# Performance work log

Measured on AMD Instinct MI355X. Metric: run time of the kernel, lower is better.

Reference implementation:

```python
import jax, jax.numpy as jnp
import numpy as np

QKV_DIM = 256
C = 32
N_HEAD = 8
OUT_DIM = 256
B1, B2, N = 1, 128, 256


def setup_inputs() -> dict:
    key = jax.random.key(0)
    ks = jax.random.split(key, 8)
    hc = N_HEAD * C
    return {
        "in_data": jax.random.normal(ks[0], (B1, B2, N, QKV_DIM), jnp.float32),
        "mask": jnp.ones((B1, B2, N), jnp.float32),
        "nonbatched_bias": jax.random.normal(ks[1], (B1, N_HEAD, N, N), jnp.float32),
        "w_qkv": jax.random.normal(ks[2], (3 * hc, QKV_DIM), jnp.float32) * (1.0 / np.sqrt(QKV_DIM)),
        "w_gate": jax.random.normal(ks[3], (hc, QKV_DIM), jnp.float32) * 0.02,
        "gating_bias": jnp.ones((hc,), jnp.float32),
        "w_o": jax.random.normal(ks[4], (OUT_DIM, hc), jnp.float32) * 0.02,
        "b_o": jnp.zeros((OUT_DIM,), jnp.float32),
    }


def reference(in_data, mask, nonbatched_bias, w_qkv, w_gate, gating_bias, w_o, b_o):
    scaling = C ** (-0.5)
    # fused QKV projection: [b1,b2,n,3*h*c]
    qkv = jnp.einsum("abnd,ed->abne", in_data, w_qkv)
    q, k, v = jnp.split(qkv, 3, axis=-1)

    def to_heads(t):  # b1 b2 n (h d) -> b1 b2 h n d
        b1, b2, n, _ = t.shape
        return t.reshape(b1, b2, n, N_HEAD, C).transpose(0, 1, 3, 2, 4)

    q, k, v = to_heads(q) * scaling, to_heads(k), to_heads(v)
    # logits: [b1,b2,h,q,k]
    logits = jnp.einsum("abhqd,abhkd->abhqk", q, k)
    mask_bias = (mask[:, :, None, None, :] - 1.0) * 1e9
    logits = logits + mask_bias + nonbatched_bias[:, None]  # broadcast bias over b2
    weights = jax.nn.softmax(logits, axis=-1)
    weighted_avg = jnp.einsum("abhqk,abhkd->abhqd", weights, v)
    b1, b2, h, n, d = weighted_avg.shape
    weighted_avg = weighted_avg.transpose(0, 1, 3, 2, 4).reshape(b1, b2, n, h * d)
    # sigmoid gating
    gate = jax.nn.sigmoid(jnp.einsum("abnd,ed->abne", in_data, w_gate) + gating_bias)
    weighted_avg = gate * weighted_avg
    return jnp.einsum("abne,oe->abno", weighted_avg, w_o) + b_o
```

## Files before the change

kernel.cpp:

```cpp
#include <hip/hip_runtime.h>
#include <hip/hip_bf16.h>
#include <math.h>

#define B2      128
#define NSEQ    256
#define DMODEL  256
#define NHEAD   8
#define CDIM    32
#define HC      256
#define NROWS   (B2*NSEQ)
#define SCALING 0.17677669529663687f

typedef __attribute__((ext_vector_type(8))) short bf16x8;
typedef __attribute__((ext_vector_type(4))) float f32x4;

static __device__ __forceinline__ ushort f2bf(float f) {
    __hip_bfloat16 b = __float2bfloat16(f);
    ushort r; __builtin_memcpy(&r, &b, 2); return r;
}
static __device__ __forceinline__ ushort f2bf_fast(float f) {
    uint u = __builtin_bit_cast(uint, f);
    return (ushort)((u + 0x8000u) >> 16);
}
static __device__ __forceinline__ uint fpack2(float a, float b) {
    const uint ua = __builtin_bit_cast(uint, a) + 0x8000u;
    const uint ub = __builtin_bit_cast(uint, b) + 0x8000u;
    return (ua >> 16) | (ub & 0xFFFF0000u);
}
static __device__ __forceinline__ float bf2f(ushort u) {
    __hip_bfloat16 b; __builtin_memcpy(&b, &u, 2); return __bfloat162float(b);
}
static __device__ __forceinline__ void gload_lds16(const void* g, void* l) {
    __builtin_amdgcn_global_load_lds((const __attribute__((address_space(1))) void*)g,
                                     (__attribute__((address_space(3))) void*)l, 16, 0, 0);
}

__global__ __launch_bounds__(256) void convertW_kernel(
    const float* __restrict__ Wqkv, const float* __restrict__ Wg,
    const float* __restrict__ Wo,
    ushort* __restrict__ wqkvgb, ushort* __restrict__ wob)
{
    const int NQ = 196608 / 4, NG = 65536 / 4, NO = 65536 / 4;
    const int idx = blockIdx.x * 256 + threadIdx.x;
    const float* src; ushort* dst; int off; float scale = 1.0f;
    if (idx < NQ)           { src = Wqkv; dst = wqkvgb;          off = idx;
                              if (off < 16384) scale = SCALING; }
    else if (idx < NQ + NG) { src = Wg;   dst = wqkvgb + 196608; off = idx - NQ; }
    else                    { src = Wo;   dst = wob;             off = idx - NQ - NG; }
    float4 v = ((const float4*)src)[off];
    union { ushort u[4]; uint2 q; } p;
    p.u[0] = f2bf(v.x * scale); p.u[1] = f2bf(v.y * scale);
    p.u[2] = f2bf(v.z * scale); p.u[3] = f2bf(v.w * scale);
    *(uint2*)(dst + (size_t)off * 4) = p.q;
}

__global__ __launch_bounds__(256) void qkvg_mfma_kernel(
    const float* __restrict__ X,
    const ushort* __restrict__ Wb,
    const float* __restrict__ gbias,
    ushort* __restrict__ q_ws,
    ushort* __restrict__ k_ws,
    ushort* __restrict__ v_ws,
    ushort* __restrict__ g_ws)
{
    __shared__ ushort S[32768];
    ushort* const Wbuf[2] = { S, S + 8192 };
    ushort* const Xls     = S + 16384;

    const int tid  = threadIdx.x;
    const int w    = tid >> 6;
    const int lane = tid & 63;
    const int lj   = lane & 15;
    const int lg   = lane >> 4;
    const int m0   = blockIdx.x * 64;

    const int srow = lane >> 2;
    const int scol = (((lane & 3) ^ ((lane >> 3) & 3)) << 3);
    const int xsl  = ((lg ^ ((lj >> 1) & 3)) << 3);

    {
        const int row  = tid >> 2;
        const int slot = tid & 3;
        const int g8   = (slot ^ ((row >> 1) & 3)) * 8;
        const float* xsrc = X + (size_t)(m0 + row) * 256 + g8;
        ushort* xdst = Xls + row * 32 + slot * 8;
        #pragma unroll
        for (int t = 0; t < 8; ++t) {
            const float4 a = *(const float4*)(xsrc + t * 32);
            const float4 b = *(const float4*)(xsrc + t * 32 + 4);
            uint4 pk;
            pk.x = fpack2(a.x, a.y); pk.y = fpack2(a.z, a.w);
            pk.z = fpack2(b.x, b.y); pk.w = fpack2(b.z, b.w);
            *(uint4*)(xdst + t * 2048) = pk;
        }
    }

    #define WSTAGE(dst, seg, kk) do {                                            \
        _Pragma("unroll")                                                        \
        for (int c = 0; c < 4; ++c) {                                            \
            const int ci = w * 4 + c;                                            \
            gload_lds16(Wb + (size_t)((seg) * 256 + ci * 16 + srow) * 256 + (kk) + scol, \
                        (char*)(dst) + ci * 1024);                               \
        } } while (0)

    const int b2 = m0 >> 8;
    const int n0 = m0 & 255;

    for (int seg = 0; seg < 4; ++seg) {
        f32x4 acc[4][4];
        #pragma unroll
        for (int i = 0; i < 4; ++i)
            #pragma unroll
            for (int j = 0; j < 4; ++j) acc[i][j] = (f32x4){0.f, 0.f, 0.f, 0.f};

        WSTAGE(Wbuf[0], seg, 0);
        __syncthreads();

        #pragma unroll
        for (int t = 0; t < 8; ++t) {
            ushort* Wc = Wbuf[t & 1];
            if (t < 7) WSTAGE(Wbuf[(t + 1) & 1], seg, (t + 1) * 32);
            bf16x8 af[4], bfr[4];
            #pragma unroll
            for (int i = 0; i < 4; ++i)
                af[i] = *(const bf16x8*)(Wc + (w * 64 + i * 16 + lj) * 32 + xsl);
            #pragma unroll
            for (int j = 0; j < 4; ++j)
                bfr[j] = *(const bf16x8*)(Xls + t * 2048 + (j * 16 + lj) * 32 + xsl);
            #pragma unroll
            for (int i = 0; i < 4; ++i)
                #pragma unroll
                for (int j = 0; j < 4; ++j)
                    acc[i][j] = __builtin_amdgcn_mfma_f32_16x16x32_bf16(af[i], bfr[j], acc[i][j], 0, 0, 0);
            asm volatile("s_waitcnt vmcnt(0)" ::: "memory");
            __builtin_amdgcn_s_barrier();
        }

        uint* T = (uint*)S;
        #pragma unroll
        for (int i = 0; i < 4; ++i) {
            const int el0 = w * 64 + i * 16 + lg * 4;
            #pragma unroll
            for (int j = 0; j < 4; ++j) {
                const int ml = j * 16 + lj;
                uint2 pk;
                if (seg == 3) {
                    float z0 = acc[i][j][0] + gbias[el0 + 0];
                    float z1 = acc[i][j][1] + gbias[el0 + 1];
                    float z2 = acc[i][j][2] + gbias[el0 + 2];
                    float z3 = acc[i][j][3] + gbias[el0 + 3];
                    pk.x = fpack2(1.f / (1.f + __expf(-z0)), 1.f / (1.f + __expf(-z1)));
                    pk.y = fpack2(1.f / (1.f + __expf(-z2)), 1.f / (1.f + __expf(-z3)));
                } else {
                    pk.x = fpack2(acc[i][j][0], acc[i][j][1]);
                    pk.y = fpack2(acc[i][j][2], acc[i][j][3]);
                }
                const int wd = (ml * 128 + (el0 >> 1)) ^ ((ml & 7) << 2);
                *(uint2*)(T + wd) = pk;
            }
        }
        __syncthreads();

        if (seg < 3) {
            ushort* base = (seg == 0) ? q_ws : (seg == 1) ? k_ws : v_ws;
            #pragma unroll
            for (int hh = 0; hh < 2; ++hh) {
                const int h = w * 2 + hh;
                ushort* gdst = base + ((size_t)(b2 * 8 + h) * 256 + n0) * 32;
                #pragma unroll
                for (int it = 0; it < 4; ++it) {
                    const int ml = it * 16 + (lane >> 2);
                    const int cq = lane & 3;
                    const int wd = (ml * 128 + h * 16 + cq * 4) ^ ((ml & 7) << 2);
                    const uint4 d = *(const uint4*)(T + wd);
                    *(uint4*)(gdst + (size_t)ml * 32 + cq * 8) = d;
                }
            }
        } else {
            const int row  = tid >> 2;
            const int part = tid & 3;
            ushort* gdst = g_ws + (size_t)(m0 + row) * 256;
            #pragma unroll
            for (int r8 = 0; r8 < 8; ++r8) {
                const int wc = r8 * 16 + part * 4;
                const int wd = (row * 128 + wc) ^ ((row & 7) << 2);
                const uint4 d = *(const uint4*)(T + wd);
                *(uint4*)(gdst + wc * 2) = d;
            }
        }
        __syncthreads();
    }
    #undef WSTAGE
}

#define SWZ(c) ((((c) >> 2) & 3) << 5)

__global__ __launch_bounds__(512) void attn_mfma_kernel(
    const ushort* __restrict__ q_ws,
    const ushort* __restrict__ k_ws,
    const ushort* __restrict__ v_ws,
    const ushort* __restrict__ g_ws,
    const float* __restrict__ bias,
    const float* __restrict__ mask,
    ushort* __restrict__ wa_ws)
{
    __shared__ ushort Ks[256 * 32];
    __shared__ ushort Vt[32 * 256];
    __shared__ ushort Pl[8 * 1024];

    const int tid  = threadIdx.x;
    const int bh   = blockIdx.x >> 1;
    const int half = blockIdx.x & 1;
    const int b2   = bh >> 3;
    const int h    = bh & 7;
    const int w    = tid >> 6;
    const int lane = tid & 63;
    const int lj   = lane & 15;
    const int lg   = lane >> 4;

    {
        const char* gk = (const char*)(k_ws + (size_t)bh * 8192);
        gload_lds16(gk + tid * 16,        (char*)Ks + w * 1024);
        gload_lds16(gk + 8192 + tid * 16, (char*)Ks + 8192 + w * 1024);
    }
    {
        const int cq = tid & 3;
        #pragma unroll
        for (int it = 0; it < 2; ++it) {
            const int n = it * 128 + (tid >> 2);
            uint4 v = *(const uint4*)(v_ws + (size_t)bh * 8192 + n * 32 + cq * 8);
            const ushort* pv = (const ushort*)&v;
            #pragma unroll
            for (int e = 0; e < 8; ++e) {
                const int c = cq * 8 + e;
                const int byte = c * 512 + ((2 * n) ^ SWZ(c));
                Vt[byte >> 1] = pv[e];
            }
        }
    }

    const int q0 = half * 128 + w * 16;
    const bf16x8 qf = *(const bf16x8*)(q_ws + (size_t)bh * 8192 + (size_t)(q0 + lj) * 32 + lg * 8);

    f32x4 acc[16];
    const float* bbase = bias + (size_t)h * 65536;
    const float* mrow  = mask + (size_t)b2 * 256;
    #pragma unroll
    for (int t = 0; t < 16; ++t) {
        const int col = t * 16 + lj;
        const float mterm = (mrow[col] - 1.0f) * 1e9f;
        #pragma unroll
        for (int r = 0; r < 4; ++r) {
            const int qrow = q0 + lg * 4 + r;
            acc[t][r] = bbase[(size_t)qrow * 256 + col] + mterm;
        }
    }

    __syncthreads();

    #pragma unroll
    for (int t = 0; t < 16; ++t) {
        const bf16x8 kf = *(const bf16x8*)(Ks + (t * 16 + lj) * 32 + lg * 8);
        acc[t] = __builtin_amdgcn_mfma_f32_16x16x32_bf16(qf, kf, acc[t], 0, 0, 0);
    }

    float s[4] = {0.f, 0.f, 0.f, 0.f};
    #pragma unroll
    for (int t = 0; t < 16; ++t)
        #pragma unroll
        for (int r = 0; r < 4; ++r) {
            const float e = __expf(acc[t][r]);
            acc[t][r] = e;
            s[r] += e;
        }
    float inv[4];
    #pragma unroll
    for (int r = 0; r < 4; ++r) {
        float sr = s[r];
        sr += __shfl_xor(sr, 1);
        sr += __shfl_xor(sr, 2);
        sr += __shfl_xor(sr, 4);
        sr += __shfl_xor(sr, 8);
        inv[r] = 1.0f / sr;
    }

    ushort* PlW = Pl + w * 1024;
    f32x4 o0 = {0.f, 0.f, 0.f, 0.f};
    f32x4 o1 = {0.f, 0.f, 0.f, 0.f};
    #pragma unroll
    for (int ch = 0; ch < 4; ++ch) {
        #pragma unroll
        for (int tt = 0; tt < 4; ++tt) {
            const int t = ch * 4 + tt;
            #pragma unroll
            for (int r = 0; r < 4; ++r) {
                const int row  = lg * 4 + r;
                const int byte = row * 128 + ((32 * tt + 2 * lj) ^ (lg << 5));
                PlW[byte >> 1] = f2bf_fast(acc[t][r]);
            }
        }
        #pragma unroll
        for (int kk = 0; kk < 2; ++kk) {
            const int abyte = lj * 128 + ((64 * kk + 16 * lg) ^ SWZ(lj));
            const bf16x8 pa = *(const bf16x8*)(PlW + (abyte >> 1));
            const int ks = ch * 2 + kk;
            {
                const int cr = lj;
                const int vbyte = cr * 512 + ((64 * ks + 16 * lg) ^ SWZ(cr));
                const bf16x8 vb = *(const bf16x8*)(Vt + (vbyte >> 1));
                o0 = __builtin_amdgcn_mfma_f32_16x16x32_bf16(pa, vb, o0, 0, 0, 0);
            }
            {
                const int cr = 16 + lj;
                const int vbyte = cr * 512 + ((64 * ks + 16 * lg) ^ SWZ(cr));
                const bf16x8 vb = *(const bf16x8*)(Vt + (vbyte >> 1));
                o1 = __builtin_amdgcn_mfma_f32_16x16x32_bf16(pa, vb, o1, 0, 0, 0);
            }
        }
    }

    #pragma unroll
    for (int r = 0; r < 4; ++r) {
        const int qrow = q0 + lg * 4 + r;
        const size_t rowbase = ((size_t)(b2 * 256 + qrow)) * 256 + h * 32;
        {
            const float gv = bf2f(g_ws[rowbase + lj]);
            wa_ws[rowbase + lj] = f2bf_fast(o0[r] * inv[r] * gv);
        }
        {
            const float gv = bf2f(g_ws[rowbase + 16 + lj]);
            wa_ws[rowbase + 16 + lj] = f2bf_fast(o1[r] * inv[r] * gv);
        }
    }
}

__global__ __launch_bounds__(256) void out_mfma_kernel(
    const ushort* __restrict__ WA,
    const ushort* __restrict__ Wob,
    const float* __restrict__ bo,
    float* __restrict__ out)
{
    __shared__ ushort S[20480];
    ushort* const Obuf[2] = { S,        S + 10240 };
    ushort* const Abuf[2] = { S + 8192, S + 18432 };

    const int tid  = threadIdx.x;
    const int w    = tid >> 6;
    const int lane = tid & 63;
    const int lj   = lane & 15;
    const int lg   = lane >> 4;
    const int m0   = blockIdx.x * 64;

    f32x4 acc[4][4];
    #pragma unroll
    for (int i = 0; i < 4; ++i)
        #pragma unroll
        for (int j = 0; j < 4; ++j) acc[i][j] = (f32x4){0.f, 0.f, 0.f, 0.f};

    const int srow = lane >> 2;
    const int scol = (((lane & 3) ^ ((lane >> 3) & 3)) << 3);
    const int xsl  = ((lg ^ ((lj >> 1) & 3)) << 3);

    #define OSTAGE(Odst, Adst, kk) do {                                          \
        _Pragma("unroll")                                                        \
        for (int c = 0; c < 4; ++c) {                                            \
            const int ci = w * 4 + c;                                            \
            gload_lds16(Wob + (size_t)(ci * 16 + srow) * 256 + (kk) + scol,      \
                        (char*)(Odst) + ci * 1024);                              \
        }                                                                        \
        gload_lds16(WA + (size_t)(m0 + w * 16 + srow) * 256 + (kk) + scol,       \
                    (char*)(Adst) + w * 1024);                                   \
    } while (0)

    OSTAGE(Obuf[0], Abuf[0], 0);
    asm volatile("s_waitcnt vmcnt(0)" ::: "memory");
    __builtin_amdgcn_s_barrier();

    #pragma unroll
    for (int t = 0; t < 8; ++t) {
        ushort* Oc = Obuf[t & 1];
        ushort* Ac = Abuf[t & 1];
        if (t < 7) OSTAGE(Obuf[(t + 1) & 1], Abuf[(t + 1) & 1], (t + 1) * 32);
        bf16x8 af[4], bfr[4];
        #pragma unroll
        for (int i = 0; i < 4; ++i)
            af[i] = *(const bf16x8*)(Ac + (i * 16 + lj) * 32 + xsl);
        #pragma unroll
        for (int j = 0; j < 4; ++j)
            bfr[j] = *(const bf16x8*)(Oc + (w * 64 + j * 16 + lj) * 32 + xsl);
        #pragma unroll
        for (int i = 0; i < 4; ++i)
            #pragma unroll
            for (int j = 0; j < 4; ++j)
                acc[i][j] = __builtin_amdgcn_mfma_f32_16x16x32_bf16(af[i], bfr[j], acc[i][j], 0, 0, 0);
        asm volatile("s_waitcnt vmcnt(0)" ::: "memory");
        __builtin_amdgcn_s_barrier();
    }
    #undef OSTAGE

    #pragma unroll
    for (int i = 0; i < 4; ++i) {
        #pragma unroll
        for (int r = 0; r < 4; ++r) {
            const int m = m0 + i * 16 + lg * 4 + r;
            #pragma unroll
            for (int j = 0; j < 4; ++j) {
                const int o = w * 64 + j * 16 + lj;
                out[(size_t)m * 256 + o] = acc[i][j][r] + bo[o];
            }
        }
    }
}

extern "C" void kernel_launch(void* const* d_in, const int* in_sizes, int n_in,
                              void* d_out, int out_size, void* d_ws, size_t ws_size,
                              hipStream_t stream) {
    const float* in_data = (const float*)d_in[0];
    const float* mask    = (const float*)d_in[1];
    const float* nb_bias = (const float*)d_in[2];
    const float* w_qkv   = (const float*)d_in[3];
    const float* w_gate  = (const float*)d_in[4];
    const float* g_bias  = (const float*)d_in[5];
    const float* w_o     = (const float*)d_in[6];
    const float* b_o     = (const float*)d_in[7];
    float* out = (float*)d_out;

    ushort* ws = (ushort*)d_ws;
    const size_t per_head = (size_t)B2 * NHEAD * NSEQ * CDIM;
    ushort* q_ws   = ws;
    ushort* k_ws   = q_ws + per_head;
    ushort* v_ws   = k_ws + per_head;
    ushort* g_ws   = v_ws + per_head;
    ushort* wa_ws  = g_ws + (size_t)NROWS * HC;
    ushort* wqkvgb = wa_ws + (size_t)NROWS * HC;
    ushort* wob    = wqkvgb + 1024 * 256;

    convertW_kernel<<<dim3(320), 256, 0, stream>>>(
        w_qkv, w_gate, w_o, wqkvgb, wob);

    qkvg_mfma_kernel<<<dim3(NROWS / 64), 256, 0, stream>>>(
        in_data, wqkvgb, g_bias, q_ws, k_ws, v_ws, g_ws);

    attn_mfma_kernel<<<dim3(B2 * NHEAD * 2), 512, 0, stream>>>(
        q_ws, k_ws, v_ws, g_ws, nb_bias, mask, wa_ws);

    out_mfma_kernel<<<dim3(NROWS / 64), 256, 0, stream>>>(
        wa_ws, wob, b_o, out);
}
```

Baseline: 93.03 us.

## Load QKVG weight fragments directly into registers and drop LDS staging barriers

The projection kernel no longer stages weight tiles through double-buffered LDS with per-step barriers. Each wave now prefetches its own weight fragments from global memory straight into registers, using a 4-deep rotating register buffer three steps ahead. The output transpose through LDS is arranged so each wave reads and writes only its own region, which lets the per-segment __syncthreads be removed. This trades LDS traffic and synchronisation for more VGPRs and uncoalesced 16-byte global loads of the weights.

```diff
diff --git a/kernel.cpp b/kernel.cpp
--- a/kernel.cpp
+++ b/kernel.cpp
@@ -64,8 +64,7 @@
     ushort* __restrict__ g_ws)
 {
     __shared__ ushort S[32768];
-    ushort* const Wbuf[2] = { S, S + 8192 };
-    ushort* const Xls     = S + 16384;
+    ushort* const Xls = S + 16384;
 
     const int tid  = threadIdx.x;
     const int w    = tid >> 6;
@@ -74,9 +73,19 @@
     const int lg   = lane >> 4;
     const int m0   = blockIdx.x * 64;
 
-    const int srow = lane >> 2;
-    const int scol = (((lane & 3) ^ ((lane >> 3) & 3)) << 3);
     const int xsl  = ((lg ^ ((lj >> 1) & 3)) << 3);
+
+    bf16x8 wf[4][4];
+    const ushort* const wbase = Wb + (size_t)(w * 64 + lj) * 256 + lg * 8;
+    #define WLOAD(s, b) do {                                                     \
+        if ((s) < 32) {                                                          \
+            const ushort* wp = wbase + (size_t)((s) >> 3) * 65536 + ((s) & 7) * 32; \
+            _Pragma("unroll")                                                    \
+            for (int i = 0; i < 4; ++i)                                          \
+                wf[b][i] = *(const bf16x8*)(wp + i * 16 * 256);                  \
+        } } while (0)
+
+    WLOAD(0, 0); WLOAD(1, 1); WLOAD(2, 2);
 
     {
         const int row  = tid >> 2;
@@ -94,17 +103,11 @@
             *(uint4*)(xdst + t * 2048) = pk;
         }
     }
-
-    #define WSTAGE(dst, seg, kk) do {                                            \
-        _Pragma("unroll")                                                        \
-        for (int c = 0; c < 4; ++c) {                                            \
-            const int ci = w * 4 + c;                                            \
-            gload_lds16(Wb + (size_t)((seg) * 256 + ci * 16 + srow) * 256 + (kk) + scol, \
-                        (char*)(dst) + ci * 1024);                               \
-        } } while (0)
+    __syncthreads();
 
     const int b2 = m0 >> 8;
     const int n0 = m0 & 255;
+    uint* T = (uint*)S;
 
     for (int seg = 0; seg < 4; ++seg) {
         f32x4 acc[4][4];
@@ -113,30 +116,21 @@
             #pragma unroll
             for (int j = 0; j < 4; ++j) acc[i][j] = (f32x4){0.f, 0.f, 0.f, 0.f};
 
-        WSTAGE(Wbuf[0], seg, 0);
-        __syncthreads();
-
-        #pragma unroll
-        for (int t = 0; t < 8; ++t) {
-            ushort* Wc = Wbuf[t & 1];
-            if (t < 7) WSTAGE(Wbuf[(t + 1) & 1], seg, (t + 1) * 32);
-            bf16x8 af[4], bfr[4];
-            #pragma unroll
-            for (int i = 0; i < 4; ++i)
-                af[i] = *(const bf16x8*)(Wc + (w * 64 + i * 16 + lj) * 32 + xsl);
+        #pragma unroll
+        for (int tt = 0; tt < 8; ++tt) {
+            const int s = seg * 8 + tt;
+            WLOAD(s + 3, (tt + 3) & 3);
+            bf16x8 bfr[4];
             #pragma unroll
             for (int j = 0; j < 4; ++j)
-                bfr[j] = *(const bf16x8*)(Xls + t * 2048 + (j * 16 + lj) * 32 + xsl);
+                bfr[j] = *(const bf16x8*)(Xls + tt * 2048 + (j * 16 + lj) * 32 + xsl);
             #pragma unroll
             for (int i = 0; i < 4; ++i)
                 #pragma unroll
                 for (int j = 0; j < 4; ++j)
-                    acc[i][j] = __builtin_amdgcn_mfma_f32_16x16x32_bf16(af[i], bfr[j], acc[i][j], 0, 0, 0);
-            asm volatile("s_waitcnt vmcnt(0)" ::: "memory");
-            __builtin_amdgcn_s_barrier();
-        }
-
-        uint* T = (uint*)S;
+                    acc[i][j] = __builtin_amdgcn_mfma_f32_16x16x32_bf16(wf[tt & 3][i], bfr[j], acc[i][j], 0, 0, 0);
+        }
+
         #pragma unroll
         for (int i = 0; i < 4; ++i) {
             const int el0 = w * 64 + i * 16 + lg * 4;
@@ -159,7 +153,6 @@
                 *(uint2*)(T + wd) = pk;
             }
         }
-        __syncthreads();
 
         if (seg < 3) {
             ushort* base = (seg == 0) ? q_ws : (seg == 1) ? k_ws : v_ws;
@@ -177,20 +170,17 @@
                 }
             }
         } else {
-            const int row  = tid >> 2;
-            const int part = tid & 3;
-            ushort* gdst = g_ws + (size_t)(m0 + row) * 256;
-            #pragma unroll
-            for (int r8 = 0; r8 < 8; ++r8) {
-                const int wc = r8 * 16 + part * 4;
-                const int wd = (row * 128 + wc) ^ ((row & 7) << 2);
+            #pragma unroll
+            for (int it = 0; it < 8; ++it) {
+                const int ml  = it * 8 + (lane >> 3);
+                const int sub = lane & 7;
+                const int wd  = (ml * 128 + w * 32 + sub * 4) ^ ((ml & 7) << 2);
                 const uint4 d = *(const uint4*)(T + wd);
-                *(uint4*)(gdst + wc * 2) = d;
-            }
-        }
-        __syncthreads();
-    }
-    #undef WSTAGE
+                *(uint4*)(g_ws + (size_t)(m0 + ml) * 256 + w * 64 + sub * 8) = d;
+            }
+        }
+    }
+    #undef WLOAD
 }
 
 #define SWZ(c) ((((c) >> 2) & 3) << 5)
```

New measurement: 107.2 us. 1.15x slower.
